# Performance work log

Measured on AMD Instinct MI355X. Metric: run time of the kernel, lower is better.

Reference implementation:

```python
import jax, jax.numpy as jnp
import numpy as np
import math

B, T, C = 2, 2048, 1024
H = 16            # n_head
RATIO = 4         # ratio_kv
HKV = H // RATIO  # n_head_kv = 4
HD = C // H       # head_dim = 64
G = H // HKV      # query heads per kv head = 4


def _alibi_slopes(n_heads):
    # n_heads must be a power of 2 here (H=16)
    assert math.log2(n_heads).is_integer()
    start = 2.0 ** (-(2.0 ** (-(math.log2(n_heads) - 3))))
    return np.array([start * (start ** i) for i in range(n_heads)], dtype=np.float32)


def setup_inputs() -> dict:
    key = jax.random.key(0)
    ks = jax.random.split(key, 5)
    return {
        "x": jax.random.normal(ks[0], (B, T, C), dtype=jnp.float32),
        "Wq": jax.random.normal(ks[1], (C, C), dtype=jnp.float32) * 0.02,
        "Wk": jax.random.normal(ks[2], (C, HKV * HD), dtype=jnp.float32) * 0.02,
        "Wv": jax.random.normal(ks[3], (C, HKV * HD), dtype=jnp.float32) * 0.02,
        "Wo": jax.random.normal(ks[4], (C, C), dtype=jnp.float32) * 0.02,
    }


def reference(x, Wq, Wk, Wv, Wo):
    # GQA causal attention with ALiBi bias (flash-disabled fallback path).
    # q: [B,HKV,G,T,HD] (grouped query heads), k/v: [B,HKV,T,HD]
    q = (x @ Wq).reshape(B, T, H, HD).transpose(0, 2, 1, 3).reshape(B, HKV, G, T, HD)
    k = (x @ Wk).reshape(B, T, HKV, HD).transpose(0, 2, 1, 3)
    v = (x @ Wv).reshape(B, T, HKV, HD).transpose(0, 2, 1, 3)

    scale = 1.0 / math.sqrt(HD)
    att = jnp.einsum('bkgtd,bksd->bkgts', q, k) * scale  # [B,HKV,G,T,T]

    # ALiBi: original repeats alibi(n_head) by G and truncates to n_head,
    # so query head h uses slope get_slopes(H)[h // G] == slopes[:HKV] per kv group.
    slopes = jnp.asarray(_alibi_slopes(H))[:HKV]          # [HKV]
    pos = jnp.arange(T)
    rel = (pos[None, :] - pos[:, None]).astype(jnp.float32)  # [T,T], rel[i,j]=j-i
    bias = slopes[:, None, None] * rel                    # [HKV,T,T]
    causal = jnp.triu(jnp.full((T, T), -jnp.inf, dtype=jnp.float32), 1)

    att = att + bias[None, :, None] + causal
    att = jax.nn.softmax(att.astype(jnp.float32), axis=-1).astype(q.dtype)

    y = jnp.einsum('bkgts,bksd->bkgtd', att, v)           # [B,HKV,G,T,HD]
    y = y.reshape(B, H, T, HD).transpose(0, 2, 1, 3).reshape(B, T, C)
    return y @ Wo
```

## Files before the change

### kernel.cpp

```cpp
#include <hip/hip_runtime.h>
#include <hip/hip_bf16.h>
#include <math.h>

#define B_ 2
#define T_ 2048
#define C_ 1024
#define H_ 16
#define HKV_ 4
#define G_ 4
#define HD_ 64
#define KVC_ 256
#define NQKV_ 1536
#define NQT_ 32

typedef __attribute__((ext_vector_type(8))) short bf16x8;
typedef __attribute__((ext_vector_type(4))) short bf16x4;
typedef __attribute__((ext_vector_type(4))) float f32x4;

static __device__ inline short f2bf(float f) {
    __hip_bfloat16 h = __float2bfloat16(f);
    short s;
    __builtin_memcpy(&s, &h, 2);
    return s;
}
static __device__ inline float bf2f(short s) {
    unsigned int u = ((unsigned int)(unsigned short)s) << 16;
    float f;
    __builtin_memcpy(&f, &u, 4);
    return f;
}
static __device__ inline bf16x4 pack4_trunc(float p0, float p1, float p2, float p3) {
    unsigned a, b, c, d;
    __builtin_memcpy(&a, &p0, 4); __builtin_memcpy(&b, &p1, 4);
    __builtin_memcpy(&c, &p2, 4); __builtin_memcpy(&d, &p3, 4);
    int2 v;
    v.x = (int)((a >> 16) | (b & 0xffff0000u));
    v.y = (int)((c >> 16) | (d & 0xffff0000u));
    return __builtin_bit_cast(bf16x4, v);
}

static __device__ inline f32x4 mfma32(bf16x8 a, bf16x8 b, f32x4 c) {
    return __builtin_amdgcn_mfma_f32_16x16x32_bf16(a, b, c, 0, 0, 0);
}
static __device__ inline f32x4 mfma16(bf16x4 a, bf16x4 b, f32x4 c) {
    return __builtin_amdgcn_mfma_f32_16x16x16bf16_1k(a, b, c, 0, 0, 0);
}

static __device__ inline void gload_lds16(const short* g, short* lds) {
    __builtin_amdgcn_global_load_lds(
        (const __attribute__((address_space(1))) unsigned int*)g,
        (__attribute__((address_space(3))) unsigned int*)lds, 16, 0, 0);
}

__global__ __launch_bounds__(256) void cast_bf16(
    const float* __restrict__ in, short* __restrict__ out, int n)
{
    const int i = (blockIdx.x * 256 + threadIdx.x) * 8;
    if (i >= n) return;
    const float4 a = *(const float4*)(in + i);
    const float4 b = *(const float4*)(in + i + 4);
    bf16x8 o;
    o[0] = f2bf(a.x); o[1] = f2bf(a.y); o[2] = f2bf(a.z); o[3] = f2bf(a.w);
    o[4] = f2bf(b.x); o[5] = f2bf(b.y); o[6] = f2bf(b.z); o[7] = f2bf(b.w);
    *(bf16x8*)(out + i) = o;
}

__global__ __launch_bounds__(256) void w_transpose(
    const float* __restrict__ Wq, const float* __restrict__ Wk,
    const float* __restrict__ Wv, const float* __restrict__ Wo,
    short* __restrict__ Wt, short* __restrict__ Wot)
{
    const int z = blockIdx.z;
    const float* in;
    short* out;
    int N;
    if (z == 0)      { in = Wq; out = Wt;                     N = C_; }
    else if (z == 1) { in = Wk; out = Wt + C_ * C_;           N = KVC_; }
    else if (z == 2) { in = Wv; out = Wt + (C_ + KVC_) * C_;  N = KVC_; }
    else             { in = Wo; out = Wot;                    N = C_; }
    const int n0 = blockIdx.x * 32;
    if (n0 >= N) return;
    __shared__ float t[32][33];
    const int tx = threadIdx.x, ty = threadIdx.y;
    const int k0 = blockIdx.y * 32;
    #pragma unroll
    for (int j = 0; j < 4; j++)
        t[ty + j * 8][tx] = in[(size_t)(k0 + ty + j * 8) * N + n0 + tx];
    __syncthreads();
    #pragma unroll
    for (int j = 0; j < 4; j++)
        out[(size_t)(n0 + ty + j * 8) * C_ + k0 + tx] = f2bf(t[tx][ty + j * 8]);
}

template <int MODE>
__global__ __launch_bounds__(256) void gemm_bf16(
    const short* __restrict__ A, const short* __restrict__ Bt,
    void* __restrict__ Cout, short* __restrict__ Ktg, short* __restrict__ Vtg,
    int M, int N, int K)
{
    __shared__ short As[64 * 32];
    __shared__ short Bs[128 * 32];
    const int tid = threadIdx.x;
    const int wave = tid >> 6, lane = tid & 63;
    const int l15 = lane & 15, quad = lane >> 4;
    const int row0 = blockIdx.y * 64, col0 = blockIdx.x * 128;
    const int wrow = (wave >> 1) * 32, wcol = (wave & 1) * 64;

    f32x4 acc[2][4];
    #pragma unroll
    for (int i = 0; i < 2; i++)
        #pragma unroll
        for (int j = 0; j < 4; j++)
            acc[i][j] = (f32x4){0.f, 0.f, 0.f, 0.f};

    for (int kt = 0; kt < K; kt += 32) {
        __syncthreads();
        {
            const int r = wave * 16 + (lane >> 2);
            const int kof = (lane & 3) * 8;
            gload_lds16(A + (size_t)(row0 + r) * K + kt + kof, &As[wave * 512]);
        }
        #pragma unroll
        for (int c2 = 0; c2 < 2; c2++) {
            const int c = wave * 2 + c2;
            const int r = c * 16 + (lane >> 2);
            const int kof = (lane & 3) * 8;
            gload_lds16(Bt + (size_t)(col0 + r) * K + kt + kof, &Bs[c * 512]);
        }
        __syncthreads();

        bf16x8 af[2], bf[4];
        #pragma unroll
        for (int mt = 0; mt < 2; mt++)
            af[mt] = *(const bf16x8*)&As[(wrow + mt * 16 + l15) * 32 + quad * 8];
        #pragma unroll
        for (int nt = 0; nt < 4; nt++)
            bf[nt] = *(const bf16x8*)&Bs[(wcol + nt * 16 + l15) * 32 + quad * 8];
        #pragma unroll
        for (int mt = 0; mt < 2; mt++)
            #pragma unroll
            for (int nt = 0; nt < 4; nt++)
                acc[mt][nt] = mfma32(af[mt], bf[nt], acc[mt][nt]);
    }

    if (MODE == 0) {
        #pragma unroll
        for (int mt = 0; mt < 2; mt++)
            #pragma unroll
            for (int r = 0; r < 4; r++) {
                const size_t row = row0 + wrow + mt * 16 + quad * 4 + r;
                #pragma unroll
                for (int nt = 0; nt < 4; nt++)
                    ((float*)Cout)[row * N + col0 + wcol + nt * 16 + l15]
                        = acc[mt][nt][r];
            }
    } else {
        if (col0 < C_) {
            #pragma unroll
            for (int mt = 0; mt < 2; mt++)
                #pragma unroll
                for (int r = 0; r < 4; r++) {
                    const size_t row = row0 + wrow + mt * 16 + quad * 4 + r;
                    #pragma unroll
                    for (int nt = 0; nt < 4; nt++)
                        ((short*)Cout)[row * N + col0 + wcol + nt * 16 + l15]
                            = f2bf(acc[mt][nt][r]);
                }
        } else if (col0 < C_ + KVC_) {
            const int kh = ((col0 - C_) >> 6) + (wcol >> 6);
            const int b = row0 >> 11, jt = (row0 & (T_ - 1)) >> 6;
            const size_t tbase = (size_t)((b * HKV_ + kh) * 32 + jt) * 4096;
            #pragma unroll
            for (int mt = 0; mt < 2; mt++)
                #pragma unroll
                for (int r = 0; r < 4; r++) {
                    const int key = wrow + mt * 16 + quad * 4 + r;
                    #pragma unroll
                    for (int nt = 0; nt < 4; nt++) {
                        const int d = nt * 16 + l15;
                        Ktg[tbase + key * 64 + (((d >> 3) ^ (key & 7)) << 3) + (d & 7)]
                            = f2bf(acc[mt][nt][r]);
                    }
                }
        } else {
            const int kh = ((col0 - C_ - KVC_) >> 6) + (wcol >> 6);
            const int b = row0 >> 11, jt = (row0 & (T_ - 1)) >> 6;
            const size_t tbase = (size_t)((b * HKV_ + kh) * 32 + jt) * 4096;
            #pragma unroll
            for (int mt = 0; mt < 2; mt++) {
                const int kblk = ((wrow + mt * 16) >> 3) + (quad >> 1);
                #pragma unroll
                for (int nt = 0; nt < 4; nt++) {
                    const int d = nt * 16 + l15;
                    bf16x4 v4;
                    v4[0] = f2bf(acc[mt][nt][0]); v4[1] = f2bf(acc[mt][nt][1]);
                    v4[2] = f2bf(acc[mt][nt][2]); v4[3] = f2bf(acc[mt][nt][3]);
                    *(bf16x4*)(Vtg + tbase + d * 64
                               + ((kblk ^ (d & 7)) << 3) + ((quad & 1) << 2)) = v4;
                }
            }
        }
    }
}

__global__ __launch_bounds__(256) void attn_mfma(
    const short* __restrict__ QKV, const short* __restrict__ Ktg,
    const short* __restrict__ Vtg, short* __restrict__ Y)
{
    const int qx = blockIdx.x;
    const int bh = blockIdx.y;
    const int qtL = qx, qtH = NQT_ - 1 - qx;
    const int b = bh >> 4, h = bh & 15, kh = h >> 2;
    const float slope2 = exp2f(-0.5f * (float)(kh + 1)) * 1.44269504f;
    const int tid = threadIdx.x;
    const int wave = tid >> 6, lane = tid & 63;
    const int l15 = lane & 15, quad = lane >> 4;
    const int lswz = (l15 & 7) * 8;

    __shared__ short Ks[4096];
    __shared__ short Vs[4096];

    const size_t bT = (size_t)b * T_;
    const size_t tb0 = (size_t)((b * HKV_ + kh) * 32) * 4096;
    const int qrow0H = qtH * 64 + wave * 16;
    const int qrow0L = qtL * 64 + wave * 16;

    const float qscale = 0.125f * 1.44269504f;
    bf16x8 qfH[2], qfL[2];
    #pragma unroll
    for (int k0 = 0; k0 < 2; k0++) {
        const short* qpH = QKV + (bT + qrow0H + l15) * NQKV_ + h * 64;
        const short* qpL = QKV + (bT + qrow0L + l15) * NQKV_ + h * 64;
        bf16x8 rH = *(const bf16x8*)(qpH + k0 * 32 + quad * 8);
        bf16x8 rL = *(const bf16x8*)(qpL + k0 * 32 + quad * 8);
        #pragma unroll
        for (int j = 0; j < 8; j++) {
            qfH[k0][j] = f2bf(bf2f(rH[j]) * qscale);
            qfL[k0][j] = f2bf(bf2f(rL[j]) * qscale);
        }
    }

    const float step = slope2 * 64.f;
    f32x4 bBH[4], bBL[4];
    #pragma unroll
    for (int mtk = 0; mtk < 4; mtk++)
        #pragma unroll
        for (int r = 0; r < 4; r++) {
            const int key0 = mtk * 16 + quad * 4 + r;
            bBH[mtk][r] = slope2 * (float)(key0 - wave * 16 - l15 - qtH * 64);
            bBL[mtk][r] = slope2 * (float)(key0 - wave * 16 - l15 - qtL * 64);
        }

    const bf16x4 ones = {(short)0x3F80, (short)0x3F80, (short)0x3F80, (short)0x3F80};

    f32x4 OaccH[4], OaccL[4], laccH, laccL;
    #pragma unroll
    for (int nt = 0; nt < 4; nt++) {
        OaccH[nt] = (f32x4){0.f, 0.f, 0.f, 0.f};
        OaccL[nt] = (f32x4){0.f, 0.f, 0.f, 0.f};
    }
    laccH = (f32x4){0.f, 0.f, 0.f, 0.f};
    laccL = (f32x4){0.f, 0.f, 0.f, 0.f};

    for (int jtk = 0; jtk <= qtH; jtk++) {
        __syncthreads();
        {
            const short* Ktile = Ktg + tb0 + (size_t)jtk * 4096;
            const short* Vtile = Vtg + tb0 + (size_t)jtk * 4096;
            #pragma unroll
            for (int i = 0; i < 2; i++) {
                const int ch = wave * 2 + i;
                gload_lds16(Ktile + ch * 512 + lane * 8, &Ks[ch * 512]);
                gload_lds16(Vtile + ch * 512 + lane * 8, &Vs[ch * 512]);
            }
        }
        __syncthreads();

        const bool doL = (jtk <= qtL);
        const float jb = step * (float)jtk;

        bf16x8 kf[8];
        #pragma unroll
        for (int mtk = 0; mtk < 4; mtk++)
            #pragma unroll
            for (int k0 = 0; k0 < 2; k0++)
                kf[mtk * 2 + k0] = *(const bf16x8*)
                    &Ks[(mtk * 16 + l15) * 64 + (((k0 * 4 + quad) * 8) ^ lswz)];

        bf16x4 pTH[4], pTL[4];
        {
            const bool diag = (jtk == qtH);
            #pragma unroll
            for (int mtk = 0; mtk < 4; mtk++) {
                const f32x4 bias = bBH[mtk] + jb;
                f32x4 a = bias;
                a = mfma32(kf[mtk * 2 + 0], qfH[0], a);
                a = mfma32(kf[mtk * 2 + 1], qfH[1], a);
                float p[4];
                #pragma unroll
                for (int r = 0; r < 4; r++) {
                    p[r] = __builtin_amdgcn_exp2f(a[r]);
                    if (diag && bias[r] > 0.f) p[r] = 0.f;
                }
                pTH[mtk] = pack4_trunc(p[0], p[1], p[2], p[3]);
                laccH = mfma16(ones, pTH[mtk], laccH);
            }
        }
        if (doL) {
            const bool diag = (jtk == qtL);
            #pragma unroll
            for (int mtk = 0; mtk < 4; mtk++) {
                const f32x4 bias = bBL[mtk] + jb;
                f32x4 a = bias;
                a = mfma32(kf[mtk * 2 + 0], qfL[0], a);
                a = mfma32(kf[mtk * 2 + 1], qfL[1], a);
                float p[4];
                #pragma unroll
                for (int r = 0; r < 4; r++) {
                    p[r] = __builtin_amdgcn_exp2f(a[r]);
                    if (diag && bias[r] > 0.f) p[r] = 0.f;
                }
                pTL[mtk] = pack4_trunc(p[0], p[1], p[2], p[3]);
                laccL = mfma16(ones, pTL[mtk], laccL);
            }
        }

        #pragma unroll
        for (int mtk = 0; mtk < 4; mtk++) {
            const int kblk = (mtk << 1) + (quad >> 1);
            #pragma unroll
            for (int nt = 0; nt < 4; nt++) {
                const bf16x4 vf = *(const bf16x4*)
                    &Vs[(nt * 16 + l15) * 64
                        + ((kblk ^ (l15 & 7)) << 3) + ((quad & 1) << 2)];
                OaccH[nt] = mfma16(vf, pTH[mtk], OaccH[nt]);
                if (doL) OaccL[nt] = mfma16(vf, pTL[mtk], OaccL[nt]);
            }
        }
    }

    {
        const float invH = 1.f / laccH[0];
        const float invL = 1.f / laccL[0];
        short* ypH = Y + (bT + qrow0H + l15) * C_ + h * 64;
        short* ypL = Y + (bT + qrow0L + l15) * C_ + h * 64;
        #pragma unroll
        for (int nt = 0; nt < 4; nt++) {
            bf16x4 oH, oL;
            #pragma unroll
            for (int r = 0; r < 4; r++) {
                oH[r] = f2bf(OaccH[nt][r] * invH);
                oL[r] = f2bf(OaccL[nt][r] * invL);
            }
            *(bf16x4*)(ypH + nt * 16 + quad * 4) = oH;
            *(bf16x4*)(ypL + nt * 16 + quad * 4) = oL;
        }
    }
}

extern "C" void kernel_launch(void* const* d_in, const int* in_sizes, int n_in,
                              void* d_out, int out_size, void* d_ws, size_t ws_size,
                              hipStream_t stream) {
    const float* x  = (const float*)d_in[0];
    const float* Wq = (const float*)d_in[1];
    const float* Wk = (const float*)d_in[2];
    const float* Wv = (const float*)d_in[3];
    const float* Wo = (const float*)d_in[4];
    float* out = (float*)d_out;

    const int M = B_ * T_;
    short* xb  = (short*)d_ws;
    short* Wt  = xb  + (size_t)M * C_;
    short* Wot = Wt  + (size_t)NQKV_ * C_;
    short* QKV = Wot + (size_t)C_ * C_;
    short* Yb  = QKV + (size_t)M * NQKV_;
    short* Ktg = Yb  + (size_t)M * C_;
    short* Vtg = Ktg + (size_t)8 * 32 * 4096;

    cast_bf16<<<dim3(M * C_ / (256 * 8)), dim3(256), 0, stream>>>(x, xb, M * C_);
    w_transpose<<<dim3(32, 32, 4), dim3(32, 8), 0, stream>>>(Wq, Wk, Wv, Wo, Wt, Wot);

    gemm_bf16<1><<<dim3(NQKV_ / 128, M / 64), dim3(256), 0, stream>>>(
        xb, Wt, QKV, Ktg, Vtg, M, NQKV_, C_);
    attn_mfma<<<dim3(NQT_ / 2, B_ * H_), dim3(256), 0, stream>>>(QKV, Ktg, Vtg, Yb);
    gemm_bf16<0><<<dim3(C_ / 128, M / 64), dim3(256), 0, stream>>>(
        Yb, Wot, out, nullptr, nullptr, M, C_, C_);
}
```

Before: 190.9 us.

## Stage P tiles through LDS to use 16x16x32 MFMA for PV and row sums

Attention probabilities are now written to a per-wave swizzled LDS buffer and reloaded in A-operand layout. This lets the PV product and the softmax denominator use the wider 16x16x32 bf16 MFMA instead of 16x16x16 ones, with V fragments loaded as 8-element vectors. The aim is to halve the MFMA instruction count for PV. In exchange it adds LDS round trips, an explicit lgkmcnt wait and extra shared memory. The output stores also become scalar 2-byte writes because the accumulator layout is transposed.

```diff
diff --git a/kernel.cpp b/kernel.cpp
--- a/kernel.cpp
+++ b/kernel.cpp
@@ -41,9 +41,6 @@
 
 static __device__ inline f32x4 mfma32(bf16x8 a, bf16x8 b, f32x4 c) {
     return __builtin_amdgcn_mfma_f32_16x16x32_bf16(a, b, c, 0, 0, 0);
-}
-static __device__ inline f32x4 mfma16(bf16x4 a, bf16x4 b, f32x4 c) {
-    return __builtin_amdgcn_mfma_f32_16x16x16bf16_1k(a, b, c, 0, 0, 0);
 }
 
 static __device__ inline void gload_lds16(const short* g, short* lds) {
@@ -203,6 +200,8 @@
     }
 }
 
+#define LSTR 72
+
 __global__ __launch_bounds__(256) void attn_mfma(
     const short* __restrict__ QKV, const short* __restrict__ Ktg,
     const short* __restrict__ Vtg, short* __restrict__ Y)
@@ -216,9 +215,12 @@
     const int wave = tid >> 6, lane = tid & 63;
     const int l15 = lane & 15, quad = lane >> 4;
     const int lswz = (l15 & 7) * 8;
+    const int pswz = l15 & 7;
 
     __shared__ short Ks[4096];
     __shared__ short Vs[4096];
+    __shared__ short Ps[4 * 32 * LSTR];
+    short* Pw = &Ps[wave * 32 * LSTR];
 
     const size_t bT = (size_t)b * T_;
     const size_t tb0 = (size_t)((b * HKV_ + kh) * 32) * 4096;
@@ -251,7 +253,8 @@
             bBL[mtk][r] = slope2 * (float)(key0 - wave * 16 - l15 - qtL * 64);
         }
 
-    const bf16x4 ones = {(short)0x3F80, (short)0x3F80, (short)0x3F80, (short)0x3F80};
+    const short one_s = (short)0x3F80;
+    const bf16x8 ones = {one_s, one_s, one_s, one_s, one_s, one_s, one_s, one_s};
 
     f32x4 OaccH[4], OaccL[4], laccH, laccL;
     #pragma unroll
@@ -287,7 +290,6 @@
                 kf[mtk * 2 + k0] = *(const bf16x8*)
                     &Ks[(mtk * 16 + l15) * 64 + (((k0 * 4 + quad) * 8) ^ lswz)];
 
-        bf16x4 pTH[4], pTL[4];
         {
             const bool diag = (jtk == qtH);
             #pragma unroll
@@ -302,8 +304,9 @@
                     p[r] = __builtin_amdgcn_exp2f(a[r]);
                     if (diag && bias[r] > 0.f) p[r] = 0.f;
                 }
-                pTH[mtk] = pack4_trunc(p[0], p[1], p[2], p[3]);
-                laccH = mfma16(ones, pTH[mtk], laccH);
+                *(bf16x4*)&Pw[l15 * LSTR
+                    + ((((mtk * 2 + (quad >> 1)) ^ pswz) << 3) | ((quad & 1) << 2))]
+                    = pack4_trunc(p[0], p[1], p[2], p[3]);
             }
         }
         if (doL) {
@@ -320,40 +323,57 @@
                     p[r] = __builtin_amdgcn_exp2f(a[r]);
                     if (diag && bias[r] > 0.f) p[r] = 0.f;
                 }
-                pTL[mtk] = pack4_trunc(p[0], p[1], p[2], p[3]);
-                laccL = mfma16(ones, pTL[mtk], laccL);
-            }
-        }
-
-        #pragma unroll
-        for (int mtk = 0; mtk < 4; mtk++) {
-            const int kblk = (mtk << 1) + (quad >> 1);
+                *(bf16x4*)&Pw[(16 + l15) * LSTR
+                    + ((((mtk * 2 + (quad >> 1)) ^ pswz) << 3) | ((quad & 1) << 2))]
+                    = pack4_trunc(p[0], p[1], p[2], p[3]);
+            }
+        }
+        __asm__ volatile("s_waitcnt lgkmcnt(0)" ::: "memory");
+
+        bf16x8 vf[8];
+        #pragma unroll
+        for (int nt = 0; nt < 4; nt++)
+            #pragma unroll
+            for (int k0 = 0; k0 < 2; k0++)
+                vf[nt * 2 + k0] = *(const bf16x8*)
+                    &Vs[(nt * 16 + l15) * 64 + (((k0 * 4 + quad) * 8) ^ lswz)];
+
+        {
+            bf16x8 pf0 = *(const bf16x8*)&Pw[l15 * LSTR + (((quad ^ pswz)) << 3)];
+            bf16x8 pf1 = *(const bf16x8*)&Pw[l15 * LSTR + (((4 + quad) ^ pswz) << 3)];
+            laccH = mfma32(pf0, ones, laccH);
+            laccH = mfma32(pf1, ones, laccH);
             #pragma unroll
             for (int nt = 0; nt < 4; nt++) {
-                const bf16x4 vf = *(const bf16x4*)
-                    &Vs[(nt * 16 + l15) * 64
-                        + ((kblk ^ (l15 & 7)) << 3) + ((quad & 1) << 2)];
-                OaccH[nt] = mfma16(vf, pTH[mtk], OaccH[nt]);
-                if (doL) OaccL[nt] = mfma16(vf, pTL[mtk], OaccL[nt]);
-            }
-        }
-    }
-
-    {
-        const float invH = 1.f / laccH[0];
-        const float invL = 1.f / laccL[0];
-        short* ypH = Y + (bT + qrow0H + l15) * C_ + h * 64;
-        short* ypL = Y + (bT + qrow0L + l15) * C_ + h * 64;
+                OaccH[nt] = mfma32(pf0, vf[nt * 2 + 0], OaccH[nt]);
+                OaccH[nt] = mfma32(pf1, vf[nt * 2 + 1], OaccH[nt]);
+            }
+        }
+        if (doL) {
+            bf16x8 pf0 = *(const bf16x8*)&Pw[(16 + l15) * LSTR + (((quad ^ pswz)) << 3)];
+            bf16x8 pf1 = *(const bf16x8*)&Pw[(16 + l15) * LSTR + (((4 + quad) ^ pswz) << 3)];
+            laccL = mfma32(pf0, ones, laccL);
+            laccL = mfma32(pf1, ones, laccL);
+            #pragma unroll
+            for (int nt = 0; nt < 4; nt++) {
+                OaccL[nt] = mfma32(pf0, vf[nt * 2 + 0], OaccL[nt]);
+                OaccL[nt] = mfma32(pf1, vf[nt * 2 + 1], OaccL[nt]);
+            }
+        }
+    }
+
+    #pragma unroll
+    for (int r = 0; r < 4; r++) {
+        const float invH = 1.f / laccH[r];
+        const float invL = 1.f / laccL[r];
+        const int rowH = qrow0H + quad * 4 + r;
+        const int rowL = qrow0L + quad * 4 + r;
+        short* ypH = Y + (bT + rowH) * C_ + h * 64 + l15;
+        short* ypL = Y + (bT + rowL) * C_ + h * 64 + l15;
         #pragma unroll
         for (int nt = 0; nt < 4; nt++) {
-            bf16x4 oH, oL;
-            #pragma unroll
-            for (int r = 0; r < 4; r++) {
-                oH[r] = f2bf(OaccH[nt][r] * invH);
-                oL[r] = f2bf(OaccL[nt][r] * invL);
-            }
-            *(bf16x4*)(ypH + nt * 16 + quad * 4) = oH;
-            *(bf16x4*)(ypL + nt * 16 + quad * 4) = oL;
+            ypH[nt * 16] = f2bf(OaccH[nt][r] * invH);
+            ypL[nt * 16] = f2bf(OaccL[nt][r] * invL);
         }
     }
 }
```

After: 177.2 us. -7.2%, faster.
